# Performance work log

Hardware: AMD Instinct MI355X
Metric: run time of the kernel (lower is better)

The kernel has to match this reference:

```python
import jax, jax.numpy as jnp
import numpy as np

BETA = 0.1       # reputation weight
GAMMA = 0.1      # load penalty weight
EXPL_C = 0.1     # UCB exploration constant
LOAD_EMA = 0.9   # load EMA alpha
TOP_K = 2
EPS = 1e-10


def setup_inputs() -> dict:
    key = jax.random.key(0)
    k1, k2, k3, k4, k5 = jax.random.split(key, 5)
    B, S, H, E = 4, 4096, 2048, 64
    return {
        "x": jax.random.normal(k1, (B, S, H), dtype=jnp.float32),
        "gate_w": jax.random.normal(k2, (E, H), dtype=jnp.float32) * (1.0 / np.sqrt(H)),
        "reputation": jax.random.normal(k3, (E,), dtype=jnp.float32),
        "loads": jax.random.uniform(k4, (E,), dtype=jnp.float32),
        "counts": jax.random.uniform(k5, (E,), dtype=jnp.float32),
        "total_decisions": 1000000,
    }


def reference(x, gate_w, reputation, loads, counts, total_decisions):
    B, S, H = x.shape
    E = gate_w.shape[0]
    x_flat = x.reshape(-1, H)                                  # [T, H]
    base_logits = jnp.einsum("th,eh->te", x_flat, gate_w)      # [T, E]

    # current_batch_assignments is None -> current_loads = expert_loads
    updated_loads = LOAD_EMA * loads + (1.0 - LOAD_EMA) * loads  # [E]

    # UCB-style exploration bonus, broadcast over tokens
    expl = EXPL_C * jnp.sqrt(jnp.log(jnp.float32(total_decisions) + 1.0) / (counts + EPS))  # [E]

    selection_scores = (base_logits
                        + BETA * reputation[None, :]
                        - GAMMA * updated_loads[None, :]
                        + expl[None, :])                        # [T, E]

    top_k_scores, top_k_indices = jax.lax.top_k(selection_scores, TOP_K)  # [T, K]
    routing_weights = jax.nn.softmax(top_k_scores, axis=-1).reshape(B, S, TOP_K)
    expert_indices = top_k_indices.reshape(B, S, TOP_K)

    # differentiable load-balancing aux loss
    router_probs = jax.nn.softmax(selection_scores.astype(jnp.float32), axis=-1)  # [T, E]
    expert_gate = jax.nn.one_hot(top_k_indices, E, dtype=jnp.float32).sum(axis=1)  # [T, E]
    tokens_per_expert = expert_gate.mean(axis=0)               # [E]
    router_prob_per_expert = router_probs.mean(axis=0)         # [E]
    aux_loss = (tokens_per_expert * router_prob_per_expert).sum() * E

    return routing_weights, expert_indices, aux_loss
```

## Files before the change

kernel.cpp:

```cpp
#include <hip/hip_runtime.h>
#include <cmath>

#define HDIM 2048
#define H4   (HDIM / 4)
#define NEXP 64
#define TTOT 16384
#define KSPLIT 2
#define KBLK (HDIM / KSPLIT)
#define NSTEP (KBLK / 32)
#define BTOK 64
#define LDS_SC 65

#define WS_PARTIAL_OFF 128
#define PARTIAL_FLOATS ((size_t)(TTOT / BTOK) * KSPLIT * BTOK * NEXP)
#define GWSZ (NEXP * HDIM)

typedef short  bf16x8 __attribute__((ext_vector_type(8)));
typedef float  f32x4  __attribute__((ext_vector_type(4)));
typedef int    i32x4  __attribute__((ext_vector_type(4)));

__device__ __forceinline__ void split8(const float4 f0, const float4 f1,
                                       bf16x8* h, bf16x8* m, bf16x8* l)
{
    const float f[8] = {f0.x, f0.y, f0.z, f0.w, f1.x, f1.y, f1.z, f1.w};
    unsigned uh[8], um[8], ul[8];
    #pragma unroll
    for (int i = 0; i < 8; ++i) {
        const unsigned u = __float_as_uint(f[i]);
        uh[i] = u & 0xffff0000u;
        const float r1 = f[i] - __uint_as_float(uh[i]);
        um[i] = __float_as_uint(r1) & 0xffff0000u;
        const float r2 = r1 - __uint_as_float(um[i]);
        ul[i] = __float_as_uint(r2) & 0xffff0000u;
    }
    i32x4 vh, vm, vl;
    #pragma unroll
    for (int j = 0; j < 4; ++j) {
        vh[j] = (int)((uh[2*j] >> 16) | uh[2*j+1]);
        vm[j] = (int)((um[2*j] >> 16) | um[2*j+1]);
        vl[j] = (int)((ul[2*j] >> 16) | ul[2*j+1]);
    }
    *h = *reinterpret_cast<bf16x8*>(&vh);
    *m = *reinterpret_cast<bf16x8*>(&vm);
    *l = *reinterpret_cast<bf16x8*>(&vl);
}

__global__ __launch_bounds__(256) void split_gw_kernel(
    const float* __restrict__ gw,
    short* __restrict__ gwh, short* __restrict__ gwm, short* __restrict__ gwl)
{
    const int g   = blockIdx.x * 256 + threadIdx.x;
    const int idx = g * 8;
    const float4 f0 = *reinterpret_cast<const float4*>(gw + idx);
    const float4 f1 = *reinterpret_cast<const float4*>(gw + idx + 4);
    bf16x8 h, m, l;
    split8(f0, f1, &h, &m, &l);
    *reinterpret_cast<bf16x8*>(gwh + idx) = h;
    *reinterpret_cast<bf16x8*>(gwm + idx) = m;
    *reinterpret_cast<bf16x8*>(gwl + idx) = l;
}

__global__ __launch_bounds__(256, 2) void router_gemm_mfma(
    const float* __restrict__ x,
    const short* __restrict__ gwh,
    const short* __restrict__ gwm,
    const short* __restrict__ gwl,
    float* __restrict__ partial)
{
    const int tid  = threadIdx.x;
    const int lane = tid & 63;
    const int quad = lane >> 4;
    const int l15  = lane & 15;
    const int w    = tid >> 6;
    const int wm   = w & 1;
    const int wn   = w >> 1;
    const int tb   = blockIdx.x;
    const int kg   = blockIdx.y;
    const int T0   = tb * BTOK;

    const float4* __restrict__ x4 = reinterpret_cast<const float4*>(x);

    size_t arow[2];
    #pragma unroll
    for (int mt = 0; mt < 2; ++mt)
        arow[mt] = (size_t)(T0 + 32 * wm + 16 * mt + l15) * H4
                 + (size_t)kg * (H4 / 2) + quad * 2;

    int brow[2];
    #pragma unroll
    for (int nt = 0; nt < 2; ++nt)
        brow[nt] = (32 * wn + 16 * nt + l15) * HDIM + kg * KBLK + quad * 8;

    f32x4 acc[2][2];
    #pragma unroll
    for (int i = 0; i < 2; ++i)
        #pragma unroll
        for (int j = 0; j < 2; ++j)
            acc[i][j] = (f32x4){0.f, 0.f, 0.f, 0.f};

    #pragma unroll 2
    for (int s = 0; s < NSTEP; ++s) {
        bf16x8 bh[2], bm[2], bl[2];
        #pragma unroll
        for (int nt = 0; nt < 2; ++nt) {
            const int o = brow[nt] + s * 32;
            bh[nt] = *reinterpret_cast<const bf16x8*>(gwh + o);
            bm[nt] = *reinterpret_cast<const bf16x8*>(gwm + o);
            bl[nt] = *reinterpret_cast<const bf16x8*>(gwl + o);
        }
        bf16x8 ah[2], am[2], al[2];
        #pragma unroll
        for (int mt = 0; mt < 2; ++mt) {
            const float4 f0 = x4[arow[mt] + (size_t)s * 8];
            const float4 f1 = x4[arow[mt] + (size_t)s * 8 + 1];
            split8(f0, f1, &ah[mt], &am[mt], &al[mt]);
        }
        #pragma unroll
        for (int mt = 0; mt < 2; ++mt)
            #pragma unroll
            for (int nt = 0; nt < 2; ++nt) {
                f32x4 c = acc[mt][nt];
                c = __builtin_amdgcn_mfma_f32_16x16x32_bf16(ah[mt], bh[nt], c, 0, 0, 0);
                c = __builtin_amdgcn_mfma_f32_16x16x32_bf16(ah[mt], bm[nt], c, 0, 0, 0);
                c = __builtin_amdgcn_mfma_f32_16x16x32_bf16(am[mt], bh[nt], c, 0, 0, 0);
                c = __builtin_amdgcn_mfma_f32_16x16x32_bf16(ah[mt], bl[nt], c, 0, 0, 0);
                c = __builtin_amdgcn_mfma_f32_16x16x32_bf16(am[mt], bm[nt], c, 0, 0, 0);
                c = __builtin_amdgcn_mfma_f32_16x16x32_bf16(al[mt], bh[nt], c, 0, 0, 0);
                acc[mt][nt] = c;
            }
    }

    float* pbase = partial + ((size_t)tb * KSPLIT + kg) * (BTOK * NEXP);
    #pragma unroll
    for (int mt = 0; mt < 2; ++mt)
        #pragma unroll
        for (int nt = 0; nt < 2; ++nt) {
            const int e = 32 * wn + 16 * nt + l15;
            #pragma unroll
            for (int r = 0; r < 4; ++r) {
                const int t_loc = 32 * wm + 16 * mt + quad * 4 + r;
                pbase[(size_t)t_loc * NEXP + e] = acc[mt][nt][r];
            }
        }
}

__global__ __launch_bounds__(256) void router_reduce(
    const float* __restrict__ partial,
    const float* __restrict__ rep,
    const float* __restrict__ loads,
    const float* __restrict__ counts,
    const int*   __restrict__ total_dec,
    float* __restrict__ out_w,
    float* __restrict__ out_idx,
    float* __restrict__ prob_acc,
    float* __restrict__ gate_acc)
{
    __shared__ float sc_s[BTOK][LDS_SC];
    __shared__ float bias_s[NEXP];
    __shared__ float m_s[BTOK], z_s[BTOK];
    __shared__ int   i1_s[BTOK], i2_s[BTOK];

    const int tid = threadIdx.x;
    const int rt  = blockIdx.x;
    const int t0  = rt * BTOK;

    if (tid < NEXP) {
        float L = logf((float)(*total_dec) + 1.0f);
        bias_s[tid] = 0.1f * rep[tid] - 0.1f * loads[tid]
                    + 0.1f * sqrtf(L / (counts[tid] + 1e-10f));
    }
    __syncthreads();

    const float* p = partial + (size_t)rt * KSPLIT * (BTOK * NEXP);
    #pragma unroll
    for (int o = 0; o < (BTOK * NEXP) / 256; ++o) {
        const int idx = o * 256 + tid;
        float s = p[idx] + p[BTOK * NEXP + idx];
        sc_s[idx >> 6][idx & 63] = s + bias_s[idx & 63];
    }
    __syncthreads();

    if (tid < BTOK) {
        const int t = tid;
        float m1 = -INFINITY, m2 = -INFINITY;
        int   i1 = 0, i2 = 0;
        for (int e = 0; e < NEXP; ++e) {
            const float s = sc_s[t][e];
            if (s > m1)      { m2 = m1; i2 = i1; m1 = s; i1 = e; }
            else if (s > m2) { m2 = s; i2 = e; }
        }
        float z = 0.0f;
        for (int e = 0; e < NEXP; ++e) z += expf(sc_s[t][e] - m1);

        const float e2  = expf(m2 - m1);
        const float inv = 1.0f / (1.0f + e2);
        const int   gt  = t0 + t;
        reinterpret_cast<float2*>(out_w)[gt]   = make_float2(inv, e2 * inv);
        reinterpret_cast<float2*>(out_idx)[gt] = make_float2((float)i1, (float)i2);
        m_s[t] = m1; z_s[t] = z; i1_s[t] = i1; i2_s[t] = i2;
    }
    __syncthreads();

    if (tid < NEXP) {
        const int e = tid;
        float ps = 0.0f, gs = 0.0f;
        for (int t = 0; t < BTOK; ++t) {
            ps += expf(sc_s[t][e] - m_s[t]) / z_s[t];
            gs += (float)((i1_s[t] == e) + (i2_s[t] == e));
        }
        atomicAdd(&prob_acc[e], ps);
        atomicAdd(&gate_acc[e], gs);
    }
}

#define BKF  32
#define LDAF (64 + 4)
__global__ __launch_bounds__(256) void router_main(
    const float* __restrict__ x,
    const float* __restrict__ gw,
    const float* __restrict__ rep,
    const float* __restrict__ loads,
    const float* __restrict__ counts,
    const int*   __restrict__ total_dec,
    float* __restrict__ out_w,
    float* __restrict__ out_idx,
    float* __restrict__ prob_acc,
    float* __restrict__ gate_acc)
{
    __shared__ float a_s[2][BKF][LDAF];
    __shared__ float b_s[2][BKF][LDAF];
    __shared__ float sc_s[64][LDS_SC];
    __shared__ float bias_s[NEXP];
    __shared__ float m_s[64], z_s[64];
    __shared__ int   i1_s[64], i2_s[64];

    const int tid = threadIdx.x;
    const int tx  = tid & 15;
    const int ty  = tid >> 4;
    const int r0  = tid >> 3;
    const int c4  = tid & 7;
    const int t0  = blockIdx.x * 64;

    if (tid < NEXP) {
        float L = logf((float)(*total_dec) + 1.0f);
        bias_s[tid] = 0.1f * rep[tid] - 0.1f * loads[tid]
                    + 0.1f * sqrtf(L / (counts[tid] + 1e-10f));
    }

    const float4* __restrict__ x4 = reinterpret_cast<const float4*>(x) + (size_t)t0 * H4;
    const float4* __restrict__ g4 = reinterpret_cast<const float4*>(gw);

    float acc[4][4] = {};

#define STORE_TILE(BUFI, A0, A1, B0, B1) do {                                  \
        float _t0[4] = {(A0).x, (A0).y, (A0).z, (A0).w};                       \
        float _t1[4] = {(A1).x, (A1).y, (A1).z, (A1).w};                       \
        float _t2[4] = {(B0).x, (B0).y, (B0).z, (B0).w};                       \
        float _t3[4] = {(B1).x, (B1).y, (B1).z, (B1).w};                       \
        _Pragma("unroll")                                                      \
        for (int u = 0; u < 4; ++u) {                                          \
            a_s[BUFI][c4 * 4 + u][r0]      = _t0[u];                           \
            a_s[BUFI][c4 * 4 + u][r0 + 32] = _t1[u];                           \
            b_s[BUFI][c4 * 4 + u][r0]      = _t2[u];                           \
            b_s[BUFI][c4 * 4 + u][r0 + 32] = _t3[u];                           \
        } } while (0)

    {
        float4 a0 = x4[(size_t)r0 * H4 + c4];
        float4 a1 = x4[(size_t)(r0 + 32) * H4 + c4];
        float4 b0 = g4[(size_t)r0 * H4 + c4];
        float4 b1 = g4[(size_t)(r0 + 32) * H4 + c4];
        STORE_TILE(0, a0, a1, b0, b1);
    }
    __syncthreads();

    int buf = 0;
    for (int it = 0; it < HDIM / BKF; ++it) {
        float4 na0, na1, nb0, nb1;
        const bool has_next = (it + 1 < HDIM / BKF);
        if (has_next) {
            const int k4 = (it + 1) * (BKF / 4);
            na0 = x4[(size_t)r0 * H4 + k4 + c4];
            na1 = x4[(size_t)(r0 + 32) * H4 + k4 + c4];
            nb0 = g4[(size_t)r0 * H4 + k4 + c4];
            nb1 = g4[(size_t)(r0 + 32) * H4 + k4 + c4];
        }
        #pragma unroll
        for (int kk = 0; kk < BKF; ++kk) {
            const float4 afv = *reinterpret_cast<const float4*>(&a_s[buf][kk][ty * 4]);
            const float4 bfv = *reinterpret_cast<const float4*>(&b_s[buf][kk][tx * 4]);
            const float af[4] = {afv.x, afv.y, afv.z, afv.w};
            const float bf[4] = {bfv.x, bfv.y, bfv.z, bfv.w};
            #pragma unroll
            for (int i = 0; i < 4; ++i)
                #pragma unroll
                for (int j = 0; j < 4; ++j)
                    acc[i][j] = fmaf(af[i], bf[j], acc[i][j]);
        }
        if (has_next) STORE_TILE(buf ^ 1, na0, na1, nb0, nb1);
        __syncthreads();
        buf ^= 1;
    }
#undef STORE_TILE

    #pragma unroll
    for (int i = 0; i < 4; ++i)
        #pragma unroll
        for (int j = 0; j < 4; ++j)
            sc_s[ty * 4 + i][tx * 4 + j] = acc[i][j] + bias_s[tx * 4 + j];
    __syncthreads();

    if (tid < 64) {
        const int t = tid;
        float m1 = -INFINITY, m2 = -INFINITY;
        int   i1 = 0, i2 = 0;
        for (int e = 0; e < NEXP; ++e) {
            const float s = sc_s[t][e];
            if (s > m1)      { m2 = m1; i2 = i1; m1 = s; i1 = e; }
            else if (s > m2) { m2 = s; i2 = e; }
        }
        float z = 0.0f;
        for (int e = 0; e < NEXP; ++e) z += expf(sc_s[t][e] - m1);
        const float e2  = expf(m2 - m1);
        const float inv = 1.0f / (1.0f + e2);
        const int   gt  = t0 + t;
        reinterpret_cast<float2*>(out_w)[gt]   = make_float2(inv, e2 * inv);
        reinterpret_cast<float2*>(out_idx)[gt] = make_float2((float)i1, (float)i2);
        m_s[t] = m1; z_s[t] = z; i1_s[t] = i1; i2_s[t] = i2;
    }
    __syncthreads();

    if (tid < NEXP) {
        const int e = tid;
        float ps = 0.0f, gs = 0.0f;
        for (int t = 0; t < 64; ++t) {
            ps += expf(sc_s[t][e] - m_s[t]) / z_s[t];
            gs += (float)((i1_s[t] == e) + (i2_s[t] == e));
        }
        atomicAdd(&prob_acc[e], ps);
        atomicAdd(&gate_acc[e], gs);
    }
}

__global__ void router_aux(const float* __restrict__ prob_acc,
                           const float* __restrict__ gate_acc,
                           float* __restrict__ out_aux)
{
    const float invT = 1.0f / (float)TTOT;
    const int e = threadIdx.x;
    float v = (gate_acc[e] * invT) * (prob_acc[e] * invT);
    #pragma unroll
    for (int off = 32; off > 0; off >>= 1)
        v += __shfl_down(v, off);
    if (e == 0) out_aux[0] = v * (float)NEXP;
}

extern "C" void kernel_launch(void* const* d_in, const int* in_sizes, int n_in,
                              void* d_out, int out_size, void* d_ws, size_t ws_size,
                              hipStream_t stream)
{
    const float* x      = (const float*)d_in[0];
    const float* gw     = (const float*)d_in[1];
    const float* rep    = (const float*)d_in[2];
    const float* loads  = (const float*)d_in[3];
    const float* counts = (const float*)d_in[4];
    const int*   total  = (const int*)d_in[5];

    float* out     = (float*)d_out;
    float* out_w   = out;
    float* out_idx = out + 32768;
    float* out_aux = out + 65536;

    float* prob_acc = (float*)d_ws;
    float* gate_acc = prob_acc + NEXP;
    float* partial  = (float*)d_ws + WS_PARTIAL_OFF;
    short* gwsplit  = (short*)((float*)d_ws + WS_PARTIAL_OFF + PARTIAL_FLOATS);
    short* gwh = gwsplit;
    short* gwm = gwsplit + GWSZ;
    short* gwl = gwsplit + 2 * GWSZ;

    const size_t ws_needed = (WS_PARTIAL_OFF + PARTIAL_FLOATS) * sizeof(float)
                           + 3 * GWSZ * sizeof(short);

    hipMemsetAsync(d_ws, 0, WS_PARTIAL_OFF * sizeof(float), stream);

    if (ws_size >= ws_needed) {
        split_gw_kernel<<<dim3(GWSZ / (256 * 8)), dim3(256), 0, stream>>>(gw, gwh, gwm, gwl);
        router_gemm_mfma<<<dim3(TTOT / BTOK, KSPLIT), dim3(256), 0, stream>>>(
            x, gwh, gwm, gwl, partial);
        router_reduce<<<dim3(TTOT / BTOK), dim3(256), 0, stream>>>(
            partial, rep, loads, counts, total, out_w, out_idx, prob_acc, gate_acc);
    } else {
        router_main<<<dim3(TTOT / 64), dim3(256), 0, stream>>>(
            x, gw, rep, loads, counts, total, out_w, out_idx, prob_acc, gate_acc);
    }
    router_aux<<<dim3(1), dim3(64), 0, stream>>>(prob_acc, gate_acc, out_aux);
}
```

Baseline: 278.7 us.

## Split K four ways and double-buffer x loads in router GEMM

Raises the K-split from 2 to 4 so twice as many blocks run the gate GEMM, and raises the occupancy hint in launch bounds to 4. The main loop is rewritten with explicit register double-buffering: the next step's x rows are loaded while the current step is split to bf16 and fed to MFMA, which is meant to hide global load latency. The reduce kernel now sums four partial slices, which doubles partial-buffer traffic and may raise register pressure under the tighter launch bound.

```diff
diff --git a/kernel.cpp b/kernel.cpp
--- a/kernel.cpp
+++ b/kernel.cpp
@@ -5,7 +5,7 @@
 #define H4   (HDIM / 4)
 #define NEXP 64
 #define TTOT 16384
-#define KSPLIT 2
+#define KSPLIT 4
 #define KBLK (HDIM / KSPLIT)
 #define NSTEP (KBLK / 32)
 #define BTOK 64
@@ -60,7 +60,7 @@
     *reinterpret_cast<bf16x8*>(gwl + idx) = l;
 }
 
-__global__ __launch_bounds__(256, 2) void router_gemm_mfma(
+__global__ __launch_bounds__(256, 4) void router_gemm_mfma(
     const float* __restrict__ x,
     const short* __restrict__ gwh,
     const short* __restrict__ gwm,
@@ -80,68 +80,86 @@
 
     const float4* __restrict__ x4 = reinterpret_cast<const float4*>(x);
 
-    size_t arow[2];
-    #pragma unroll
-    for (int mt = 0; mt < 2; ++mt)
-        arow[mt] = (size_t)(T0 + 32 * wm + 16 * mt + l15) * H4
-                 + (size_t)kg * (H4 / 2) + quad * 2;
-
-    int brow[2];
-    #pragma unroll
-    for (int nt = 0; nt < 2; ++nt)
-        brow[nt] = (32 * wn + 16 * nt + l15) * HDIM + kg * KBLK + quad * 8;
-
-    f32x4 acc[2][2];
-    #pragma unroll
-    for (int i = 0; i < 2; ++i)
-        #pragma unroll
-        for (int j = 0; j < 2; ++j)
-            acc[i][j] = (f32x4){0.f, 0.f, 0.f, 0.f};
-
-    #pragma unroll 2
-    for (int s = 0; s < NSTEP; ++s) {
-        bf16x8 bh[2], bm[2], bl[2];
-        #pragma unroll
-        for (int nt = 0; nt < 2; ++nt) {
-            const int o = brow[nt] + s * 32;
-            bh[nt] = *reinterpret_cast<const bf16x8*>(gwh + o);
-            bm[nt] = *reinterpret_cast<const bf16x8*>(gwm + o);
-            bl[nt] = *reinterpret_cast<const bf16x8*>(gwl + o);
-        }
-        bf16x8 ah[2], am[2], al[2];
-        #pragma unroll
-        for (int mt = 0; mt < 2; ++mt) {
-            const float4 f0 = x4[arow[mt] + (size_t)s * 8];
-            const float4 f1 = x4[arow[mt] + (size_t)s * 8 + 1];
-            split8(f0, f1, &ah[mt], &am[mt], &al[mt]);
-        }
-        #pragma unroll
-        for (int mt = 0; mt < 2; ++mt)
-            #pragma unroll
-            for (int nt = 0; nt < 2; ++nt) {
-                f32x4 c = acc[mt][nt];
-                c = __builtin_amdgcn_mfma_f32_16x16x32_bf16(ah[mt], bh[nt], c, 0, 0, 0);
-                c = __builtin_amdgcn_mfma_f32_16x16x32_bf16(ah[mt], bm[nt], c, 0, 0, 0);
-                c = __builtin_amdgcn_mfma_f32_16x16x32_bf16(am[mt], bh[nt], c, 0, 0, 0);
-                c = __builtin_amdgcn_mfma_f32_16x16x32_bf16(ah[mt], bl[nt], c, 0, 0, 0);
-                c = __builtin_amdgcn_mfma_f32_16x16x32_bf16(am[mt], bm[nt], c, 0, 0, 0);
-                c = __builtin_amdgcn_mfma_f32_16x16x32_bf16(al[mt], bh[nt], c, 0, 0, 0);
-                acc[mt][nt] = c;
-            }
-    }
+    const size_t arow0 = (size_t)(T0 + 32 * wm + l15) * H4
+                       + (size_t)kg * (H4 / KSPLIT) + quad * 2;
+    const size_t arow1 = arow0 + (size_t)16 * H4;
+
+    const int brow0 = (32 * wn + l15) * HDIM + kg * KBLK + quad * 8;
+    const int brow1 = brow0 + 16 * HDIM;
+
+    f32x4 acc00 = {0.f,0.f,0.f,0.f}, acc01 = {0.f,0.f,0.f,0.f};
+    f32x4 acc10 = {0.f,0.f,0.f,0.f}, acc11 = {0.f,0.f,0.f,0.f};
+
+    float4 p00, p01, p02, p03;
+    float4 q00, q01, q02, q03;
+
+#define LOADA(S, R0, R1, R2, R3) do {                                          \
+        R0 = x4[arow0 + (size_t)(S) * 8];                                      \
+        R1 = x4[arow0 + (size_t)(S) * 8 + 1];                                  \
+        R2 = x4[arow1 + (size_t)(S) * 8];                                      \
+        R3 = x4[arow1 + (size_t)(S) * 8 + 1];                                  \
+    } while (0)
+
+#define COMPUTE(S, R0, R1, R2, R3) do {                                        \
+        const int _o0 = brow0 + (S) * 32;                                      \
+        const int _o1 = brow1 + (S) * 32;                                      \
+        const bf16x8 bh0 = *reinterpret_cast<const bf16x8*>(gwh + _o0);        \
+        const bf16x8 bh1 = *reinterpret_cast<const bf16x8*>(gwh + _o1);        \
+        const bf16x8 bm0 = *reinterpret_cast<const bf16x8*>(gwm + _o0);        \
+        const bf16x8 bm1 = *reinterpret_cast<const bf16x8*>(gwm + _o1);        \
+        const bf16x8 bl0 = *reinterpret_cast<const bf16x8*>(gwl + _o0);        \
+        const bf16x8 bl1 = *reinterpret_cast<const bf16x8*>(gwl + _o1);        \
+        bf16x8 ah0, am0, al0, ah1, am1, al1;                                   \
+        split8(R0, R1, &ah0, &am0, &al0);                                      \
+        split8(R2, R3, &ah1, &am1, &al1);                                      \
+        acc00 = __builtin_amdgcn_mfma_f32_16x16x32_bf16(ah0, bh0, acc00, 0,0,0);\
+        acc00 = __builtin_amdgcn_mfma_f32_16x16x32_bf16(ah0, bm0, acc00, 0,0,0);\
+        acc00 = __builtin_amdgcn_mfma_f32_16x16x32_bf16(am0, bh0, acc00, 0,0,0);\
+        acc00 = __builtin_amdgcn_mfma_f32_16x16x32_bf16(ah0, bl0, acc00, 0,0,0);\
+        acc00 = __builtin_amdgcn_mfma_f32_16x16x32_bf16(am0, bm0, acc00, 0,0,0);\
+        acc00 = __builtin_amdgcn_mfma_f32_16x16x32_bf16(al0, bh0, acc00, 0,0,0);\
+        acc01 = __builtin_amdgcn_mfma_f32_16x16x32_bf16(ah0, bh1, acc01, 0,0,0);\
+        acc01 = __builtin_amdgcn_mfma_f32_16x16x32_bf16(ah0, bm1, acc01, 0,0,0);\
+        acc01 = __builtin_amdgcn_mfma_f32_16x16x32_bf16(am0, bh1, acc01, 0,0,0);\
+        acc01 = __builtin_amdgcn_mfma_f32_16x16x32_bf16(ah0, bl1, acc01, 0,0,0);\
+        acc01 = __builtin_amdgcn_mfma_f32_16x16x32_bf16(am0, bm1, acc01, 0,0,0);\
+        acc01 = __builtin_amdgcn_mfma_f32_16x16x32_bf16(al0, bh1, acc01, 0,0,0);\
+        acc10 = __builtin_amdgcn_mfma_f32_16x16x32_bf16(ah1, bh0, acc10, 0,0,0);\
+        acc10 = __builtin_amdgcn_mfma_f32_16x16x32_bf16(ah1, bm0, acc10, 0,0,0);\
+        acc10 = __builtin_amdgcn_mfma_f32_16x16x32_bf16(am1, bh0, acc10, 0,0,0);\
+        acc10 = __builtin_amdgcn_mfma_f32_16x16x32_bf16(ah1, bl0, acc10, 0,0,0);\
+        acc10 = __builtin_amdgcn_mfma_f32_16x16x32_bf16(am1, bm0, acc10, 0,0,0);\
+        acc10 = __builtin_amdgcn_mfma_f32_16x16x32_bf16(al1, bh0, acc10, 0,0,0);\
+        acc11 = __builtin_amdgcn_mfma_f32_16x16x32_bf16(ah1, bh1, acc11, 0,0,0);\
+        acc11 = __builtin_amdgcn_mfma_f32_16x16x32_bf16(ah1, bm1, acc11, 0,0,0);\
+        acc11 = __builtin_amdgcn_mfma_f32_16x16x32_bf16(am1, bh1, acc11, 0,0,0);\
+        acc11 = __builtin_amdgcn_mfma_f32_16x16x32_bf16(ah1, bl1, acc11, 0,0,0);\
+        acc11 = __builtin_amdgcn_mfma_f32_16x16x32_bf16(am1, bm1, acc11, 0,0,0);\
+        acc11 = __builtin_amdgcn_mfma_f32_16x16x32_bf16(al1, bh1, acc11, 0,0,0);\
+    } while (0)
+
+    LOADA(0, p00, p01, p02, p03);
+
+    #pragma unroll
+    for (int s = 0; s < NSTEP; s += 2) {
+        if (s + 1 < NSTEP) LOADA(s + 1, q00, q01, q02, q03);
+        COMPUTE(s, p00, p01, p02, p03);
+        if (s + 2 < NSTEP) LOADA(s + 2, p00, p01, p02, p03);
+        COMPUTE(s + 1, q00, q01, q02, q03);
+    }
+#undef LOADA
+#undef COMPUTE
 
     float* pbase = partial + ((size_t)tb * KSPLIT + kg) * (BTOK * NEXP);
-    #pragma unroll
-    for (int mt = 0; mt < 2; ++mt)
-        #pragma unroll
-        for (int nt = 0; nt < 2; ++nt) {
-            const int e = 32 * wn + 16 * nt + l15;
-            #pragma unroll
-            for (int r = 0; r < 4; ++r) {
-                const int t_loc = 32 * wm + 16 * mt + quad * 4 + r;
-                pbase[(size_t)t_loc * NEXP + e] = acc[mt][nt][r];
-            }
-        }
+    const int e0 = 32 * wn + l15;
+    #pragma unroll
+    for (int r = 0; r < 4; ++r) {
+        const int tr0 = 32 * wm + quad * 4 + r;
+        pbase[(size_t)tr0 * NEXP + e0]             = acc00[r];
+        pbase[(size_t)tr0 * NEXP + e0 + 16]        = acc01[r];
+        pbase[(size_t)(tr0 + 16) * NEXP + e0]      = acc10[r];
+        pbase[(size_t)(tr0 + 16) * NEXP + e0 + 16] = acc11[r];
+    }
 }
 
 __global__ __launch_bounds__(256) void router_reduce(
@@ -175,7 +193,10 @@
     #pragma unroll
     for (int o = 0; o < (BTOK * NEXP) / 256; ++o) {
         const int idx = o * 256 + tid;
-        float s = p[idx] + p[BTOK * NEXP + idx];
+        float s = 0.0f;
+        #pragma unroll
+        for (int g = 0; g < KSPLIT; ++g)
+            s += p[(size_t)g * (BTOK * NEXP) + idx];
         sc_s[idx >> 6][idx & 63] = s + bias_s[idx & 63];
     }
     __syncthreads();
```

New measurement: 272.5 us. -2.2%, faster.
